# Kernel optimization log

Measured on AMD Instinct MI355X. Metric: run time of the kernel, lower is better.

The kernel has to match this reference:

```python
import jax, jax.numpy as jnp
import numpy as np
import math

D = 1024
H = 16
DH = D // H
FF = 4096
B, S = 2, 2048


def _layernorm(x, g, b, eps=1e-5):
    mu = jnp.mean(x, axis=-1, keepdims=True)
    var = jnp.var(x, axis=-1, keepdims=True)
    return (x - mu) * jax.lax.rsqrt(var + eps) * g + b


def _gelu_tanh(x):
    # 0.5*x*(1+tanh(sqrt(2/pi)*(x+0.044715*x^3)))
    c = math.sqrt(2.0 / math.pi)
    return 0.5 * x * (1.0 + jnp.tanh(c * (x + 0.044715 * x ** 3)))


def setup_inputs() -> dict:
    key = jax.random.key(0)
    ks = jax.random.split(key, 8)
    s = 0.02
    return {
        "x": jax.random.normal(ks[0], (B, S, D), dtype=jnp.float32),
        "ln1_g": jnp.ones((D,), jnp.float32),
        "ln1_b": jnp.zeros((D,), jnp.float32),
        "Wqkv": jax.random.normal(ks[1], (D, 3 * D), jnp.float32) * s,
        "bqkv": jnp.zeros((3 * D,), jnp.float32),
        "Wo": jax.random.normal(ks[2], (D, D), jnp.float32) * s,
        "bo": jnp.zeros((D,), jnp.float32),
        "ln2_g": jnp.ones((D,), jnp.float32),
        "ln2_b": jnp.zeros((D,), jnp.float32),
        "W1": jax.random.normal(ks[3], (D, FF), jnp.float32) * s,
        "b1": jnp.zeros((FF,), jnp.float32),
        "W2": jax.random.normal(ks[4], (FF, D), jnp.float32) * s,
        "b2": jnp.zeros((D,), jnp.float32),
    }


def reference(x, ln1_g, ln1_b, Wqkv, bqkv, Wo, bo, ln2_g, ln2_b, W1, b1, W2, b2):
    b, s, d = x.shape
    h = _layernorm(x, ln1_g, ln1_b)
    qkv = h @ Wqkv + bqkv                       # [B,S,3D]
    q, k, v = jnp.split(qkv, 3, axis=-1)
    q = q.reshape(b, s, H, DH).transpose(0, 2, 1, 3)   # [B,H,S,Dh]
    k = k.reshape(b, s, H, DH).transpose(0, 2, 1, 3)
    v = v.reshape(b, s, H, DH).transpose(0, 2, 1, 3)
    scores = jnp.einsum("bhqd,bhkd->bhqk", q, k) / math.sqrt(DH)
    probs = jax.nn.softmax(scores, axis=-1)
    attn = jnp.einsum("bhqk,bhkd->bhqd", probs, v)     # [B,H,S,Dh]
    attn = attn.transpose(0, 2, 1, 3).reshape(b, s, d)
    attn = attn @ Wo + bo
    x = x + attn
    m = _layernorm(x, ln2_g, ln2_b)
    m = _gelu_tanh(m @ W1 + b1) @ W2 + b2
    return x + m
```

## Files before the change

kernel.cpp:

```cpp
#include <hip/hip_runtime.h>
#include <hip/hip_bf16.h>
#include <cstdint>

#define D_ 1024
#define H_ 16
#define DH_ 64
#define FF_ 4096
#define B_ 2
#define S_ 2048
#define MR_ (B_ * S_)

typedef __bf16 bf16x8 __attribute__((ext_vector_type(8)));
typedef __bf16 bf16x4 __attribute__((ext_vector_type(4)));
typedef float f32x4 __attribute__((ext_vector_type(4)));
typedef float f32x16 __attribute__((ext_vector_type(16)));

__device__ __forceinline__ void g2lds16(const void* g, void* l) {
  __builtin_amdgcn_global_load_lds(
      (__attribute__((address_space(1))) void*)(uintptr_t)g,
      (__attribute__((address_space(3))) void*)(uint32_t)(uintptr_t)l,
      16, 0, 0);
}

__device__ __forceinline__ unsigned pkbf16(float lo, float hi) {
  unsigned r;
  asm("v_cvt_pk_bf16_f32 %0, %1, %2" : "=v"(r) : "v"(lo), "v"(hi));
  return r;
}

__device__ __forceinline__ float max3f(float a, float b, float c) {
  float d;
  asm("v_max3_f32 %0, %1, %2, %3" : "=v"(d) : "v"(a), "v"(b), "v"(c));
  return d;
}

__device__ __forceinline__ float rmax16(const f32x16& v) {
  float t0 = max3f(v[0], v[1], v[2]);
  float t1 = max3f(v[3], v[4], v[5]);
  float t2 = max3f(v[6], v[7], v[8]);
  float t3 = max3f(v[9], v[10], v[11]);
  float t4 = max3f(v[12], v[13], v[14]);
  return fmaxf(max3f(t0, t1, t2), max3f(t3, t4, v[15]));
}

__global__ __launch_bounds__(256) void transpose_cvt(
    const float* __restrict__ W, __hip_bfloat16* __restrict__ Wt, int K, int N) {
  __shared__ float t[32][33];
  int bx = blockIdx.x * 32;
  int by = blockIdx.y * 32;
  int tx = threadIdx.x, ty = threadIdx.y;
#pragma unroll
  for (int i = 0; i < 4; ++i)
    t[ty + 8 * i][tx] = W[(size_t)(by + ty + 8 * i) * N + bx + tx];
  __syncthreads();
#pragma unroll
  for (int i = 0; i < 4; ++i)
    Wt[(size_t)(bx + ty + 8 * i) * K + by + tx] = __float2bfloat16(t[tx][ty + 8 * i]);
}

__global__ __launch_bounds__(256) void transpose_v(
    const __hip_bfloat16* __restrict__ qkv, __hip_bfloat16* __restrict__ vT) {
  __shared__ __hip_bfloat16 t[32][33];
  int bh = blockIdx.z, b = bh >> 4, h = bh & 15;
  int s0 = blockIdx.x * 32, d0 = blockIdx.y * 32;
  int tx = threadIdx.x, ty = threadIdx.y;
#pragma unroll
  for (int i = 0; i < 4; ++i)
    t[ty + 8 * i][tx] =
        qkv[(size_t)(b * S_ + s0 + ty + 8 * i) * (3 * D_) + 2 * D_ + h * DH_ + d0 + tx];
  __syncthreads();
#pragma unroll
  for (int i = 0; i < 4; ++i)
    vT[(size_t)(bh * DH_ + d0 + ty + 8 * i) * S_ + s0 + tx] = t[tx][ty + 8 * i];
}

__global__ __launch_bounds__(256) void ln_kernel(
    const float* __restrict__ x, const float* __restrict__ g,
    const float* __restrict__ b, __hip_bfloat16* __restrict__ out) {
  int row = blockIdx.x;
  const float4* xr = (const float4*)(x + (size_t)row * D_);
  float4 v = xr[threadIdx.x];
  float s = v.x + v.y + v.z + v.w;
  float ss = v.x * v.x + v.y * v.y + v.z * v.z + v.w * v.w;
#pragma unroll
  for (int m = 1; m < 64; m <<= 1) {
    s += __shfl_xor(s, m);
    ss += __shfl_xor(ss, m);
  }
  __shared__ float rs[4], rss[4];
  int wave = threadIdx.x >> 6, lane = threadIdx.x & 63;
  if (lane == 0) { rs[wave] = s; rss[wave] = ss; }
  __syncthreads();
  s = rs[0] + rs[1] + rs[2] + rs[3];
  ss = rss[0] + rss[1] + rss[2] + rss[3];
  float mean = s * (1.0f / D_);
  float var = ss * (1.0f / D_) - mean * mean;
  float inv = rsqrtf(var + 1e-5f);
  int c = threadIdx.x * 4;
  float4 gv = ((const float4*)g)[threadIdx.x];
  float4 bv = ((const float4*)b)[threadIdx.x];
  __hip_bfloat16* o = out + (size_t)row * D_ + c;
  o[0] = __float2bfloat16((v.x - mean) * inv * gv.x + bv.x);
  o[1] = __float2bfloat16((v.y - mean) * inv * gv.y + bv.y);
  o[2] = __float2bfloat16((v.z - mean) * inv * gv.z + bv.z);
  o[3] = __float2bfloat16((v.w - mean) * inv * gv.w + bv.w);
}

template <int EPI>
__global__ __launch_bounds__(512) void gemm3(
    const __hip_bfloat16* __restrict__ A, const __hip_bfloat16* __restrict__ Bt,
    const float* __restrict__ bias, const float* __restrict__ resid,
    void* __restrict__ outp, int M, int N, int K) {
  constexpr int BM = 128, BN = 128, MF = 4, NF = 2, WN = 4;
  __shared__ alignas(16) __hip_bfloat16 sA[2][BM * 64];
  __shared__ alignas(16) __hip_bfloat16 sB[2][BN * 64];
  const int tid = threadIdx.x;
  const int lane = tid & 63, wave = tid >> 6;
  const int l15 = lane & 15, l4 = lane >> 4;
  const int wr = wave / WN, wc = wave % WN;
  const int csw = (l15 & 7) << 3;

  const int gx = gridDim.x;
  int nwg = gx * gridDim.y;
  int flat = blockIdx.y * gx + blockIdx.x;
  int cpx = nwg >> 3;
  int swz = (flat & 7) * cpx + (flat >> 3);
  const int m0 = (swz / gx) * BM, n0 = (swz % gx) * BN;

  f32x4 z = {0.f, 0.f, 0.f, 0.f};
  f32x4 acc[MF][NF];
#pragma unroll
  for (int i = 0; i < MF; ++i)
#pragma unroll
    for (int j = 0; j < NF; ++j) acc[i][j] = z;

  auto stage = [&](int bu, int kt) {
#pragma unroll
    for (int it = 0; it < 2; ++it) {
      int idx = it * 512 + tid;
      int r = idx >> 3, c = (idx & 7) * 8;
      int cs = c ^ ((r & 7) << 3);
      g2lds16(A + (size_t)(m0 + r) * K + kt + cs, (void*)(&sA[bu][idx * 8]));
      g2lds16(Bt + (size_t)(n0 + r) * K + kt + cs, (void*)(&sB[bu][idx * 8]));
    }
  };

  const int nk = K / 64;
  stage(0, 0);
  asm volatile("s_waitcnt vmcnt(0)" ::: "memory");
  __builtin_amdgcn_s_barrier();

  for (int j = 0; j < nk; ++j) {
    const int cur = j & 1;
    if (j + 1 < nk) stage(cur ^ 1, (j + 1) * 64);

    __builtin_amdgcn_s_setprio(1);
#pragma unroll
    for (int kk = 0; kk < 2; ++kk) {
      bf16x8 bfr[NF];
      int col = (kk * 32 + l4 * 8) ^ csw;
#pragma unroll
      for (int nf = 0; nf < NF; ++nf)
        bfr[nf] = *(const bf16x8*)(&sB[cur][(wc * NF * 16 + nf * 16 + l15) * 64 + col]);
#pragma unroll
      for (int mf = 0; mf < MF; ++mf) {
        bf16x8 af = *(const bf16x8*)(&sA[cur][(wr * MF * 16 + mf * 16 + l15) * 64 + col]);
#pragma unroll
        for (int nf = 0; nf < NF; ++nf)
          acc[mf][nf] =
              __builtin_amdgcn_mfma_f32_16x16x32_bf16(af, bfr[nf], acc[mf][nf], 0, 0, 0);
      }
    }
    __builtin_amdgcn_s_setprio(0);

    asm volatile("s_waitcnt lgkmcnt(0)" ::: "memory");
    __builtin_amdgcn_sched_barrier(0);
    asm volatile("s_waitcnt vmcnt(0)" ::: "memory");
    __builtin_amdgcn_s_barrier();
    asm volatile("" ::: "memory");
  }

#pragma unroll
  for (int mf = 0; mf < MF; ++mf) {
#pragma unroll
    for (int nf = 0; nf < NF; ++nf) {
      int col = n0 + wc * NF * 16 + nf * 16 + l15;
      float bv = bias[col];
#pragma unroll
      for (int j = 0; j < 4; ++j) {
        int row = m0 + wr * MF * 16 + mf * 16 + l4 * 4 + j;
        size_t o = (size_t)row * N + col;
        float v = acc[mf][nf][j] + bv;
        if (EPI == 0) {
          ((__hip_bfloat16*)outp)[o] = __float2bfloat16(v);
        } else if (EPI == 1) {
          ((float*)outp)[o] = v + resid[o];
        } else {
          float a = 0.7978845608028654f * (v + 0.044715f * v * v * v);
          a = fminf(fmaxf(a, -15.f), 15.f);
          float e = __expf(2.f * a);
          float th = (e - 1.f) / (e + 1.f);
          ((__hip_bfloat16*)outp)[o] = __float2bfloat16(0.5f * v * (1.f + th));
        }
      }
    }
  }
}

__global__ __launch_bounds__(256) void attn_kernel(
    const __hip_bfloat16* __restrict__ qkv, const __hip_bfloat16* __restrict__ vT,
    __hip_bfloat16* __restrict__ out) {
  __shared__ alignas(16) __hip_bfloat16 sK[2][64 * 64];
  __shared__ alignas(16) __hip_bfloat16 sV[2][64 * 64];
  __shared__ float sBr[4][32];
  const int tid = threadIdx.x, lane = tid & 63, wave = tid >> 6;
  const int l31 = lane & 31, hi = lane >> 5;
  const int bh = blockIdx.y, b = bh >> 4, h = bh & 15;
  const int q0 = blockIdx.x * 128;
  const int rsw = (l31 & 7) << 3;
  const float k2 = 0.125f * 1.44269504f;

  bf16x8 qf[4];
  {
    int qr = q0 + wave * 32 + l31;
    const size_t qbase = ((size_t)(b * S_ + qr)) * (3 * D_) + h * DH_;
#pragma unroll
    for (int ks = 0; ks < 4; ++ks) {
      bf16x8 q = *(const bf16x8*)(qkv + qbase + ks * 16 + hi * 8);
#pragma unroll
      for (int i = 0; i < 8; ++i) q[i] = (__bf16)((float)q[i] * k2);
      qf[ks] = q;
    }
  }

  bf16x8 onesb;
#pragma unroll
  for (int i = 0; i < 8; ++i) onesb[i] = (__bf16)1.0f;

  f32x16 acc0, acc1, accL;
#pragma unroll
  for (int r = 0; r < 16; ++r) { acc0[r] = 0.f; acc1[r] = 0.f; accL[r] = 0.f; }
  float mrun = -1e30f;

  const __hip_bfloat16* kg = qkv + (size_t)b * S_ * (3 * D_) + D_ + h * DH_;
  const __hip_bfloat16* vg = vT + (size_t)bh * DH_ * S_;

  auto stage = [&](int bu, int kv0) {
#pragma unroll
    for (int it = 0; it < 2; ++it) {
      int idx = it * 256 + tid;
      int r = idx >> 3;
      int c = (idx & 7) * 8;
      int cs = c ^ ((r & 7) << 3);
      g2lds16(kg + (size_t)(kv0 + r) * (3 * D_) + cs, (void*)(&sK[bu][idx * 8]));
      g2lds16(vg + (size_t)r * S_ + kv0 + cs, (void*)(&sV[bu][idx * 8]));
    }
  };

  stage(0, 0);
  const int NT = S_ / 64;

  for (int t = 0; t < NT; ++t) {
    const int cur = t & 1;
    __syncthreads();
    if (t + 1 < NT) stage(cur ^ 1, (t + 1) * 64);

    f32x16 sf0, sf1;
#pragma unroll
    for (int r = 0; r < 16; ++r) { sf0[r] = 0.f; sf1[r] = 0.f; }
    __builtin_amdgcn_s_setprio(1);
#pragma unroll
    for (int ks = 0; ks < 4; ++ks) {
      int colsw = (ks * 16 + hi * 8) ^ rsw;
      bf16x8 kf0 = *(const bf16x8*)(&sK[cur][l31 * 64 + colsw]);
      bf16x8 kf1 = *(const bf16x8*)(&sK[cur][(32 + l31) * 64 + colsw]);
      sf0 = __builtin_amdgcn_mfma_f32_32x32x16_bf16(kf0, qf[ks], sf0, 0, 0, 0);
      sf1 = __builtin_amdgcn_mfma_f32_32x32x16_bf16(kf1, qf[ks], sf1, 0, 0, 0);
    }
    __builtin_amdgcn_s_setprio(0);

    float pm = fmaxf(rmax16(sf0), rmax16(sf1));
    if (!__all(pm - mrun <= 8.0f)) {
      float mf = fmaxf(pm, __shfl_xor(pm, 32));
      float mn = fmaxf(mrun, mf);
      float corrl = exp2f(mrun - mn);
      mrun = mn;
      sBr[wave][l31] = corrl;
#pragma unroll
      for (int r = 0; r < 16; ++r) {
        float cr = sBr[wave][(r & 3) + 8 * (r >> 2) + 4 * hi];
        acc0[r] *= cr;
        acc1[r] *= cr;
        accL[r] *= cr;
      }
    }

    bf16x8 pa[4];
#pragma unroll
    for (int kb = 0; kb < 2; ++kb) {
      const f32x16 s16 = kb ? sf1 : sf0;
#pragma unroll
      for (int ksb = 0; ksb < 2; ++ksb) {
        float p0 = exp2f(s16[8 * ksb + 0] - mrun);
        float p1 = exp2f(s16[8 * ksb + 1] - mrun);
        float p2 = exp2f(s16[8 * ksb + 2] - mrun);
        float p3 = exp2f(s16[8 * ksb + 3] - mrun);
        float p4 = exp2f(s16[8 * ksb + 4] - mrun);
        float p5 = exp2f(s16[8 * ksb + 5] - mrun);
        float p6 = exp2f(s16[8 * ksb + 6] - mrun);
        float p7 = exp2f(s16[8 * ksb + 7] - mrun);
        unsigned wa = pkbf16(p0, p1), wb = pkbf16(p2, p3);
        unsigned wc = pkbf16(p4, p5), wd = pkbf16(p6, p7);
        auto r1 = __builtin_amdgcn_permlane32_swap(wa, wc, false, false);
        auto r2 = __builtin_amdgcn_permlane32_swap(wb, wd, false, false);
        union { unsigned u[4]; bf16x8 v; } w;
        w.u[0] = r1[0]; w.u[1] = r2[0]; w.u[2] = r1[1]; w.u[3] = r2[1];
        pa[kb * 2 + ksb] = w.v;
      }
    }

    __builtin_amdgcn_s_setprio(1);
#pragma unroll
    for (int ksg = 0; ksg < 4; ++ksg) {
      int colsw = (ksg * 16 + hi * 8) ^ rsw;
      bf16x8 vf0 = *(const bf16x8*)(&sV[cur][l31 * 64 + colsw]);
      bf16x8 vf1 = *(const bf16x8*)(&sV[cur][(32 + l31) * 64 + colsw]);
      acc0 = __builtin_amdgcn_mfma_f32_32x32x16_bf16(pa[ksg], vf0, acc0, 0, 0, 0);
      acc1 = __builtin_amdgcn_mfma_f32_32x32x16_bf16(pa[ksg], vf1, acc1, 0, 0, 0);
      accL = __builtin_amdgcn_mfma_f32_32x32x16_bf16(pa[ksg], onesb, accL, 0, 0, 0);
    }
    __builtin_amdgcn_s_setprio(0);
  }

#pragma unroll
  for (int r = 0; r < 16; ++r) {
    int qrow = (r & 3) + 8 * (r >> 2) + 4 * hi;
    float ir = 1.0f / accL[r];
    size_t obase = ((size_t)(b * S_ + q0 + wave * 32 + qrow)) * D_ + h * DH_ + l31;
    out[obase] = __float2bfloat16(acc0[r] * ir);
    out[obase + 32] = __float2bfloat16(acc1[r] * ir);
  }
}

extern "C" void kernel_launch(void* const* d_in, const int* in_sizes, int n_in,
                              void* d_out, int out_size, void* d_ws, size_t ws_size,
                              hipStream_t stream) {
  const float* x = (const float*)d_in[0];
  const float* ln1_g = (const float*)d_in[1];
  const float* ln1_b = (const float*)d_in[2];
  const float* Wqkv = (const float*)d_in[3];
  const float* bqkv = (const float*)d_in[4];
  const float* Wo = (const float*)d_in[5];
  const float* bo = (const float*)d_in[6];
  const float* ln2_g = (const float*)d_in[7];
  const float* ln2_b = (const float*)d_in[8];
  const float* W1 = (const float*)d_in[9];
  const float* b1 = (const float*)d_in[10];
  const float* W2 = (const float*)d_in[11];
  const float* b2 = (const float*)d_in[12];
  float* out = (float*)d_out;

  char* ws = (char*)d_ws;
  size_t off = 0;
  auto alloc = [&](size_t bytes) {
    void* p = ws + off;
    off += (bytes + 255) & ~(size_t)255;
    return p;
  };
  __hip_bfloat16* WqkvT = (__hip_bfloat16*)alloc((size_t)3 * D_ * D_ * 2);
  __hip_bfloat16* WoT = (__hip_bfloat16*)alloc((size_t)D_ * D_ * 2);
  __hip_bfloat16* W1T = (__hip_bfloat16*)alloc((size_t)FF_ * D_ * 2);
  __hip_bfloat16* W2T = (__hip_bfloat16*)alloc((size_t)D_ * FF_ * 2);
  __hip_bfloat16* h = (__hip_bfloat16*)alloc((size_t)MR_ * D_ * 2);
  __hip_bfloat16* qkv = (__hip_bfloat16*)alloc((size_t)MR_ * FF_ * 2);
  __hip_bfloat16* ff = qkv;
  __hip_bfloat16* vT = (__hip_bfloat16*)alloc((size_t)B_ * H_ * DH_ * S_ * 2);
  __hip_bfloat16* attn_out = (__hip_bfloat16*)alloc((size_t)MR_ * D_ * 2);

  dim3 tb(32, 8);
  transpose_cvt<<<dim3(3 * D_ / 32, D_ / 32), tb, 0, stream>>>(Wqkv, WqkvT, D_, 3 * D_);
  transpose_cvt<<<dim3(D_ / 32, D_ / 32), tb, 0, stream>>>(Wo, WoT, D_, D_);
  transpose_cvt<<<dim3(FF_ / 32, D_ / 32), tb, 0, stream>>>(W1, W1T, D_, FF_);
  transpose_cvt<<<dim3(D_ / 32, FF_ / 32), tb, 0, stream>>>(W2, W2T, FF_, D_);
  ln_kernel<<<MR_, 256, 0, stream>>>(x, ln1_g, ln1_b, h);
  gemm3<0><<<dim3(3 * D_ / 128, MR_ / 128), 512, 0, stream>>>(
      h, WqkvT, bqkv, nullptr, qkv, MR_, 3 * D_, D_);
  transpose_v<<<dim3(S_ / 32, DH_ / 32, B_ * H_), tb, 0, stream>>>(qkv, vT);
  attn_kernel<<<dim3(S_ / 128, B_ * H_), 256, 0, stream>>>(qkv, vT, attn_out);
  gemm3<1><<<dim3(D_ / 128, MR_ / 128), 512, 0, stream>>>(
      attn_out, WoT, bo, x, out, MR_, D_, D_);
  ln_kernel<<<MR_, 256, 0, stream>>>(out, ln2_g, ln2_b, h);
  gemm3<2><<<dim3(FF_ / 128, MR_ / 128), 512, 0, stream>>>(
      h, W1T, b1, nullptr, ff, MR_, FF_, D_);
  gemm3<1><<<dim3(D_ / 128, MR_ / 128), 512, 0, stream>>>(
      ff, W2T, b2, out, out, MR_, D_, FF_);
}
```

Before: 234.7 us.

## Split attention KV across two blocks, add 4-wave GEMM and triple-buffered GEMM

```diff
diff --git a/kernel.cpp b/kernel.cpp
--- a/kernel.cpp
+++ b/kernel.cpp
@@ -9,6 +9,7 @@
 #define B_ 2
 #define S_ 2048
 #define MR_ (B_ * S_)
+#define BHS_ (B_ * H_ * S_)
 
 typedef __bf16 bf16x8 __attribute__((ext_vector_type(8)));
 typedef __bf16 bf16x4 __attribute__((ext_vector_type(4)));
@@ -107,17 +108,17 @@
 }
 
 template <int EPI>
-__global__ __launch_bounds__(512) void gemm3(
+__global__ __launch_bounds__(256) void gemm4(
     const __hip_bfloat16* __restrict__ A, const __hip_bfloat16* __restrict__ Bt,
     const float* __restrict__ bias, const float* __restrict__ resid,
     void* __restrict__ outp, int M, int N, int K) {
-  constexpr int BM = 128, BN = 128, MF = 4, NF = 2, WN = 4;
+  constexpr int BM = 128, BN = 128, MF = 4, NF = 4;
   __shared__ alignas(16) __hip_bfloat16 sA[2][BM * 64];
   __shared__ alignas(16) __hip_bfloat16 sB[2][BN * 64];
   const int tid = threadIdx.x;
   const int lane = tid & 63, wave = tid >> 6;
   const int l15 = lane & 15, l4 = lane >> 4;
-  const int wr = wave / WN, wc = wave % WN;
+  const int wr = wave >> 1, wc = wave & 1;
   const int csw = (l15 & 7) << 3;
 
   const int gx = gridDim.x;
@@ -136,6 +137,107 @@
 
   auto stage = [&](int bu, int kt) {
 #pragma unroll
+    for (int it = 0; it < 4; ++it) {
+      int idx = it * 256 + tid;
+      int r = idx >> 3, c = (idx & 7) * 8;
+      int cs = c ^ ((r & 7) << 3);
+      g2lds16(A + (size_t)(m0 + r) * K + kt + cs, (void*)(&sA[bu][idx * 8]));
+      g2lds16(Bt + (size_t)(n0 + r) * K + kt + cs, (void*)(&sB[bu][idx * 8]));
+    }
+  };
+
+  const int nk = K / 64;
+  stage(0, 0);
+  asm volatile("s_waitcnt vmcnt(0)" ::: "memory");
+  __builtin_amdgcn_s_barrier();
+
+  for (int j = 0; j < nk; ++j) {
+    const int cur = j & 1;
+    if (j + 1 < nk) stage(cur ^ 1, (j + 1) * 64);
+
+    __builtin_amdgcn_s_setprio(1);
+#pragma unroll
+    for (int kk = 0; kk < 2; ++kk) {
+      int col = (kk * 32 + l4 * 8) ^ csw;
+      bf16x8 bfr[NF];
+#pragma unroll
+      for (int nf = 0; nf < NF; ++nf)
+        bfr[nf] = *(const bf16x8*)(&sB[cur][(wc * 64 + nf * 16 + l15) * 64 + col]);
+#pragma unroll
+      for (int mf = 0; mf < MF; ++mf) {
+        bf16x8 af = *(const bf16x8*)(&sA[cur][(wr * 64 + mf * 16 + l15) * 64 + col]);
+#pragma unroll
+        for (int nf = 0; nf < NF; ++nf)
+          acc[mf][nf] =
+              __builtin_amdgcn_mfma_f32_16x16x32_bf16(af, bfr[nf], acc[mf][nf], 0, 0, 0);
+      }
+    }
+    __builtin_amdgcn_s_setprio(0);
+
+    asm volatile("s_waitcnt lgkmcnt(0)" ::: "memory");
+    __builtin_amdgcn_sched_barrier(0);
+    asm volatile("s_waitcnt vmcnt(0)" ::: "memory");
+    __builtin_amdgcn_s_barrier();
+    asm volatile("" ::: "memory");
+  }
+
+#pragma unroll
+  for (int mf = 0; mf < MF; ++mf) {
+#pragma unroll
+    for (int nf = 0; nf < NF; ++nf) {
+      int col = n0 + wc * 64 + nf * 16 + l15;
+      float bv = bias[col];
+#pragma unroll
+      for (int j = 0; j < 4; ++j) {
+        int row = m0 + wr * 64 + mf * 16 + l4 * 4 + j;
+        size_t o = (size_t)row * N + col;
+        float v = acc[mf][nf][j] + bv;
+        if (EPI == 0) {
+          ((__hip_bfloat16*)outp)[o] = __float2bfloat16(v);
+        } else if (EPI == 1) {
+          ((float*)outp)[o] = v + resid[o];
+        } else {
+          float a = 0.7978845608028654f * (v + 0.044715f * v * v * v);
+          a = fminf(fmaxf(a, -15.f), 15.f);
+          float e = __expf(2.f * a);
+          float th = (e - 1.f) / (e + 1.f);
+          ((__hip_bfloat16*)outp)[o] = __float2bfloat16(0.5f * v * (1.f + th));
+        }
+      }
+    }
+  }
+}
+
+template <int EPI>
+__global__ __launch_bounds__(512) void gemmr3(
+    const __hip_bfloat16* __restrict__ A, const __hip_bfloat16* __restrict__ Bt,
+    const float* __restrict__ bias, const float* __restrict__ resid,
+    void* __restrict__ outp, int M, int N, int K) {
+  constexpr int BM = 128, BN = 128, MF = 4, NF = 2, WN = 4;
+  __shared__ alignas(16) __hip_bfloat16 sA[3][BM * 64];
+  __shared__ alignas(16) __hip_bfloat16 sB[3][BN * 64];
+  const int tid = threadIdx.x;
+  const int lane = tid & 63, wave = tid >> 6;
+  const int l15 = lane & 15, l4 = lane >> 4;
+  const int wr = wave / WN, wc = wave % WN;
+  const int csw = (l15 & 7) << 3;
+
+  const int gx = gridDim.x;
+  int nwg = gx * gridDim.y;
+  int flat = blockIdx.y * gx + blockIdx.x;
+  int cpx = nwg >> 3;
+  int swz = (flat & 7) * cpx + (flat >> 3);
+  const int m0 = (swz / gx) * BM, n0 = (swz % gx) * BN;
+
+  f32x4 z = {0.f, 0.f, 0.f, 0.f};
+  f32x4 acc[MF][NF];
+#pragma unroll
+  for (int i = 0; i < MF; ++i)
+#pragma unroll
+    for (int j = 0; j < NF; ++j) acc[i][j] = z;
+
+  auto stage = [&](int bu, int kt) {
+#pragma unroll
     for (int it = 0; it < 2; ++it) {
       int idx = it * 512 + tid;
       int r = idx >> 3, c = (idx & 7) * 8;
@@ -147,24 +249,26 @@
 
   const int nk = K / 64;
   stage(0, 0);
-  asm volatile("s_waitcnt vmcnt(0)" ::: "memory");
+  stage(1, 64);
+  asm volatile("s_waitcnt vmcnt(4)" ::: "memory");
   __builtin_amdgcn_s_barrier();
 
+  int bu = 0, bu2 = 2;
   for (int j = 0; j < nk; ++j) {
-    const int cur = j & 1;
-    if (j + 1 < nk) stage(cur ^ 1, (j + 1) * 64);
+    const bool pf = (j + 2) < nk;
+    if (pf) stage(bu2, (j + 2) * 64);
 
     __builtin_amdgcn_s_setprio(1);
 #pragma unroll
     for (int kk = 0; kk < 2; ++kk) {
+      int col = (kk * 32 + l4 * 8) ^ csw;
       bf16x8 bfr[NF];
-      int col = (kk * 32 + l4 * 8) ^ csw;
 #pragma unroll
       for (int nf = 0; nf < NF; ++nf)
-        bfr[nf] = *(const bf16x8*)(&sB[cur][(wc * NF * 16 + nf * 16 + l15) * 64 + col]);
+        bfr[nf] = *(const bf16x8*)(&sB[bu][(wc * NF * 16 + nf * 16 + l15) * 64 + col]);
 #pragma unroll
       for (int mf = 0; mf < MF; ++mf) {
-        bf16x8 af = *(const bf16x8*)(&sA[cur][(wr * MF * 16 + mf * 16 + l15) * 64 + col]);
+        bf16x8 af = *(const bf16x8*)(&sA[bu][(wr * MF * 16 + mf * 16 + l15) * 64 + col]);
 #pragma unroll
         for (int nf = 0; nf < NF; ++nf)
           acc[mf][nf] =
@@ -175,9 +279,14 @@
 
     asm volatile("s_waitcnt lgkmcnt(0)" ::: "memory");
     __builtin_amdgcn_sched_barrier(0);
-    asm volatile("s_waitcnt vmcnt(0)" ::: "memory");
+    if (pf)
+      asm volatile("s_waitcnt vmcnt(4)" ::: "memory");
+    else
+      asm volatile("s_waitcnt vmcnt(0)" ::: "memory");
     __builtin_amdgcn_s_barrier();
     asm volatile("" ::: "memory");
+    bu = (bu == 2) ? 0 : bu + 1;
+    bu2 = (bu2 == 2) ? 0 : bu2 + 1;
   }
 
 #pragma unroll
@@ -209,7 +318,7 @@
 
 __global__ __launch_bounds__(256) void attn_kernel(
     const __hip_bfloat16* __restrict__ qkv, const __hip_bfloat16* __restrict__ vT,
-    __hip_bfloat16* __restrict__ out) {
+    __hip_bfloat16* __restrict__ opart, float* __restrict__ Mb, float* __restrict__ Lb) {
   __shared__ alignas(16) __hip_bfloat16 sK[2][64 * 64];
   __shared__ alignas(16) __hip_bfloat16 sV[2][64 * 64];
   __shared__ float sBr[4][32];
@@ -217,6 +326,7 @@
   const int l31 = lane & 31, hi = lane >> 5;
   const int bh = blockIdx.y, b = bh >> 4, h = bh & 15;
   const int q0 = blockIdx.x * 128;
+  const int kvh = blockIdx.z;
   const int rsw = (l31 & 7) << 3;
   const float k2 = 0.125f * 1.44269504f;
 
@@ -257,13 +367,14 @@
     }
   };
 
-  stage(0, 0);
-  const int NT = S_ / 64;
+  const int NT = S_ / 128;
+  const int t0 = kvh * NT;
+  stage(0, t0 * 64);
 
   for (int t = 0; t < NT; ++t) {
     const int cur = t & 1;
     __syncthreads();
-    if (t + 1 < NT) stage(cur ^ 1, (t + 1) * 64);
+    if (t + 1 < NT) stage(cur ^ 1, (t0 + t + 1) * 64);
 
     f32x16 sf0, sf1;
 #pragma unroll
@@ -332,14 +443,42 @@
     __builtin_amdgcn_s_setprio(0);
   }
 
+  __hip_bfloat16* op = opart + (size_t)kvh * MR_ * D_;
+  float* Mp = Mb + (size_t)kvh * BHS_ + (size_t)bh * S_;
+  float* Lp = Lb + (size_t)kvh * BHS_ + (size_t)bh * S_;
 #pragma unroll
   for (int r = 0; r < 16; ++r) {
     int qrow = (r & 3) + 8 * (r >> 2) + 4 * hi;
-    float ir = 1.0f / accL[r];
     size_t obase = ((size_t)(b * S_ + q0 + wave * 32 + qrow)) * D_ + h * DH_ + l31;
-    out[obase] = __float2bfloat16(acc0[r] * ir);
-    out[obase + 32] = __float2bfloat16(acc1[r] * ir);
-  }
+    op[obase] = __float2bfloat16(acc0[r]);
+    op[obase + 32] = __float2bfloat16(acc1[r]);
+    if (l31 == 0) Lp[q0 + wave * 32 + qrow] = accL[r];
+  }
+  if (hi == 0) Mp[q0 + wave * 32 + l31] = mrun;
+}
+
+__global__ __launch_bounds__(256) void attn_combine(
+    const __hip_bfloat16* __restrict__ op, const float* __restrict__ Mb,
+    const float* __restrict__ Lb, __hip_bfloat16* __restrict__ out) {
+  size_t base = ((size_t)blockIdx.x * 256 + threadIdx.x) * 4;
+  int d = (int)(base & (D_ - 1));
+  int srow = (int)(base >> 10);
+  int h = d >> 6;
+  int b = srow >> 11;
+  int s = srow & (S_ - 1);
+  size_t ml = (size_t)(b * H_ + h) * S_ + s;
+  float m0 = Mb[ml], m1 = Mb[ml + BHS_];
+  float l0 = Lb[ml], l1 = Lb[ml + BHS_];
+  float m = fmaxf(m0, m1);
+  float w0 = exp2f(m0 - m), w1 = exp2f(m1 - m);
+  float invl = 1.0f / (l0 * w0 + l1 * w1);
+  bf16x4 o0 = *(const bf16x4*)(op + base);
+  bf16x4 o1 = *(const bf16x4*)(op + base + (size_t)MR_ * D_);
+  bf16x4 ov;
+#pragma unroll
+  for (int j = 0; j < 4; ++j)
+    ov[j] = (__bf16)(((float)o0[j] * w0 + (float)o1[j] * w1) * invl);
+  *(bf16x4*)(out + base) = ov;
 }
 
 extern "C" void kernel_launch(void* const* d_in, const int* in_sizes, int n_in,
@@ -376,6 +515,9 @@
   __hip_bfloat16* ff = qkv;
   __hip_bfloat16* vT = (__hip_bfloat16*)alloc((size_t)B_ * H_ * DH_ * S_ * 2);
   __hip_bfloat16* attn_out = (__hip_bfloat16*)alloc((size_t)MR_ * D_ * 2);
+  __hip_bfloat16* opart = (__hip_bfloat16*)alloc((size_t)2 * MR_ * D_ * 2);
+  float* Mb = (float*)alloc((size_t)2 * BHS_ * 4);
+  float* Lb = (float*)alloc((size_t)2 * BHS_ * 4);
 
   dim3 tb(32, 8);
   transpose_cvt<<<dim3(3 * D_ / 32, D_ / 32), tb, 0, stream>>>(Wqkv, WqkvT, D_, 3 * D_);
@@ -383,15 +525,16 @@
   transpose_cvt<<<dim3(FF_ / 32, D_ / 32), tb, 0, stream>>>(W1, W1T, D_, FF_);
   transpose_cvt<<<dim3(D_ / 32, FF_ / 32), tb, 0, stream>>>(W2, W2T, FF_, D_);
   ln_kernel<<<MR_, 256, 0, stream>>>(x, ln1_g, ln1_b, h);
-  gemm3<0><<<dim3(3 * D_ / 128, MR_ / 128), 512, 0, stream>>>(
+  gemm4<0><<<dim3(3 * D_ / 128, MR_ / 128), 256, 0, stream>>>(
       h, WqkvT, bqkv, nullptr, qkv, MR_, 3 * D_, D_);
   transpose_v<<<dim3(S_ / 32, DH_ / 32, B_ * H_), tb, 0, stream>>>(qkv, vT);
-  attn_kernel<<<dim3(S_ / 128, B_ * H_), 256, 0, stream>>>(qkv, vT, attn_out);
-  gemm3<1><<<dim3(D_ / 128, MR_ / 128), 512, 0, stream>>>(
+  attn_kernel<<<dim3(S_ / 128, B_ * H_, 2), 256, 0, stream>>>(qkv, vT, opart, Mb, Lb);
+  attn_combine<<<dim3(MR_ * D_ / 1024), 256, 0, stream>>>(opart, Mb, Lb, attn_out);
+  gemmr3<1><<<dim3(D_ / 128, MR_ / 128), 512, 0, stream>>>(
       attn_out, WoT, bo, x, out, MR_, D_, D_);
   ln_kernel<<<MR_, 256, 0, stream>>>(out, ln2_g, ln2_b, h);
-  gemm3<2><<<dim3(FF_ / 128, MR_ / 128), 512, 0, stream>>>(
+  gemm4<2><<<dim3(FF_ / 128, MR_ / 128), 256, 0, stream>>>(
       h, W1T, b1, nullptr, ff, MR_, FF_, D_);
-  gemm3<1><<<dim3(D_ / 128, MR_ / 128), 512, 0, stream>>>(
+  gemmr3<1><<<dim3(D_ / 128, MR_ / 128), 512, 0, stream>>>(
       ff, W2T, b2, out, out, MR_, D_, FF_);
 }
```

Result: slower. 240.0 us (+2.3%).
